# Performance work log

Measured on AMD Instinct MI355X. Metric: run time of the kernel, lower is better.

The kernel has to match this reference:

```python
import jax, jax.numpy as jnp
import numpy as np

# Dimensions (see shape_source): n_head == M == 8 is required by the module's own reshapes.
H = 8       # n_head
M = 8       # hardcoded M (must equal n_head)
D = 1024    # input_dim
E = 1024    # embed_dim
V = 128     # v_dim = embed_dim // n_head
KD = 128    # k_dim = v_dim
S = 10      # global seq_len == n_query (forced by delta_proj in-features)
K = 3       # K_num sampling points
HI, WI = 16, 16   # h_img, w_img feature-map size
BN = 4      # batch_n = batch_size // (h*w)
B = BN * HI * WI  # 1024
BNM = BN * M      # 32


def setup_inputs() -> dict:
    key = jax.random.key(0)
    ks = jax.random.split(key, 7)
    sc = 0.02
    return {
        "q": jax.random.normal(ks[0], (B, S, D), jnp.float32),
        "Wq": jax.random.normal(ks[1], (H, D, KD), jnp.float32) * sc,
        "Wk": jax.random.normal(ks[2], (H, D, KD), jnp.float32) * sc,
        "Wv": jax.random.normal(ks[3], (H, D, V * K), jnp.float32) * sc,
        "Wo": jax.random.normal(ks[4], (H, V, E), jnp.float32) * sc,
        "dw": jax.random.normal(ks[5], (2 * K * S, V * S), jnp.float32) * 0.01,
        "db": jax.random.uniform(ks[6], (2 * K * S,), jnp.float32, -1.0, 1.0),
    }


def _grid_sample_bilinear(feats, gx, gy):
    # Replicates F.grid_sample(mode='bilinear', padding_mode='zeros', align_corners=False)
    # feats: (N, h, w, S, V); gx, gy: (N, h, w, S, K) normalized grid coords in [-1, 1]-space
    n, h, w = feats.shape[0], feats.shape[1], feats.shape[2]
    ix = ((gx + 1.0) * w - 1.0) * 0.5  # unnormalize, align_corners=False
    iy = ((gy + 1.0) * h - 1.0) * 0.5
    x0 = jnp.floor(ix); y0 = jnp.floor(iy)
    x1 = x0 + 1.0;      y1 = y0 + 1.0
    wx1 = ix - x0; wx0 = 1.0 - wx1
    wy1 = iy - y0; wy0 = 1.0 - wy1
    b_idx = jnp.arange(n)[:, None, None, None, None]
    s_idx = jnp.arange(feats.shape[3])[None, None, None, :, None]

    def corner(xc, yc, wgt):
        xi = jnp.clip(xc.astype(jnp.int32), 0, w - 1)
        yi = jnp.clip(yc.astype(jnp.int32), 0, h - 1)
        valid = (xc >= 0) & (xc <= w - 1) & (yc >= 0) & (yc <= h - 1)
        val = feats[b_idx, yi, xi, s_idx]  # (N, h, w, S, K, V)
        return val * (wgt * valid)[..., None]

    return (corner(x0, y0, wx0 * wy0) + corner(x1, y0, wx1 * wy0)
            + corner(x0, y1, wx0 * wy1) + corner(x1, y1, wx1 * wy1))


def _l2norm_dim1(x):
    # F.normalize(x, p=2, dim=1) with eps=1e-12 (normalizes over the h axis)
    n = jnp.sqrt(jnp.sum(x * x, axis=1, keepdims=True))
    return x / jnp.maximum(n, 1e-12)


def _forward(q, Wq, Wk, Wv, Wo, dw, db):
    hf = q.reshape(-1, D)                                    # [B*S, D] (h defaults to q)
    qp = jnp.einsum('nd,hdk->hnk', hf, Wq).reshape(H, B, S, KD)
    kp = jnp.einsum('nd,hdk->hnk', hf, Wk).reshape(H, B, S, KD)
    vp = jnp.einsum('nd,hdk->hnk', hf, Wv).reshape(H, B, S * K, V)

    # torch: q.permute(1,2,3,0).contiguous().view(H, B, -1)  (memory reinterpretation)
    q2 = jnp.transpose(qp, (1, 2, 3, 0)).reshape(H, B, S * KD)

    deltas = (q2 @ dw.T + db).reshape(BNM, HI, WI, S, K, 2)

    gy, gx = jnp.meshgrid(jnp.arange(HI) / (HI - 1), jnp.arange(WI) / (WI - 1), indexing='ij')
    ref = jnp.stack((gx, gy), axis=-1).astype(q.dtype)        # (h, w, 2)

    pd = ref[None, :, :, None, None, :] + deltas              # (BNM, h, w, S, K, 2)
    vgx = _l2norm_dim1(pd[..., 0])
    vgy = _l2norm_dim1(pd[..., 1])

    feats = kp.reshape(BNM, HI, WI, S, V)                     # torch view of (H,B,S,k)
    samp = _grid_sample_bilinear(feats, vgx, vgy)             # (BNM, h, w, S, K, V)
    # torch stacks loop results at index k*S + s on a trailing dim, then permutes channels last
    samp = jnp.transpose(samp, (0, 1, 2, 4, 3, 5)).reshape(BNM, HI, WI, K * S, V)
    k_attn = samp.reshape(M, B, K * S, V)

    q_attn = q2.reshape(M, B, S, V)
    qk = jnp.einsum('mbqv,mbkv->mbqk', q_attn, k_attn) * (1.0 / np.sqrt(KD))
    attn = jax.nn.softmax(qk, axis=-1)                        # (M, B, S, K*S)
    attn_map = attn.mean(axis=0)[:, 0]                        # (B, K*S)

    head = jnp.einsum('mbqk,mbkv->mbqv', attn, vp)            # (M, B, S, V)
    head_flat = jnp.transpose(head, (1, 2, 0, 3)).reshape(B * S, H * V)
    out = (head_flat @ Wo.reshape(H * V, E)).reshape(B, S, E)
    return out, attn_map


def reference(q, Wq, Wk, Wv, Wo, dw, db):
    return _forward(q, Wq, Wk, Wv, Wo, dw, db)
```

## Files before the change

kernel.cpp:

```cpp
#include <hip/hip_runtime.h>


typedef float    f32x4 __attribute__((ext_vector_type(4)));
typedef short    s16x8 __attribute__((ext_vector_type(8)));
typedef unsigned short u16x8 __attribute__((ext_vector_type(8)));
typedef unsigned short u16;

__device__ __forceinline__ u16 f2bf(float f) {
  union { float f; unsigned u; } x; x.f = f;
  unsigned r = x.u + 0x7FFFu + ((x.u >> 16) & 1u);
  return (u16)(r >> 16);
}
__device__ __forceinline__ float bf2f(u16 u) {
  union { unsigned u; float f; } x; x.u = ((unsigned)u) << 16;
  return x.f;
}

#define ASYNC16(g, l) __builtin_amdgcn_global_load_lds(                       \
    (const __attribute__((address_space(1))) void*)(g),                       \
    (__attribute__((address_space(3))) void*)(l), 16, 0, 0)

__global__ __launch_bounds__(256) void conv_a(
    const float* __restrict__ src, u16* __restrict__ dst, int n8)
{
  int i = blockIdx.x * 256 + threadIdx.x;
  if (i >= n8) return;
  const float4* s = (const float4*)src + (size_t)i * 2;
  float4 a = s[0], b = s[1];
  u16x8 o;
  o[0] = f2bf(a.x); o[1] = f2bf(a.y); o[2] = f2bf(a.z); o[3] = f2bf(a.w);
  o[4] = f2bf(b.x); o[5] = f2bf(b.y); o[6] = f2bf(b.z); o[7] = f2bf(b.w);
  *(u16x8*)(dst + (size_t)i * 8) = o;
}

__global__ __launch_bounds__(256) void conv_w(
    const float* __restrict__ Wq, const float* __restrict__ Wk,
    const float* __restrict__ Wv, const float* __restrict__ Wo,
    u16* __restrict__ Wcat)
{
  int i = blockIdx.x * 256 + threadIdx.x;
  if (i >= 6144 * 128) return;
  int c = i >> 7;
  int d0 = (i & 127) * 8;
  const float* src; int stride;
  if (c < 1024)      { int kq = c >> 3, h = c & 7;
                       src = Wq + (size_t)h * 131072 + kq;      stride = 128; }
  else if (c < 2048) { int j = c - 1024; int h = j >> 7, k = j & 127;
                       src = Wk + (size_t)h * 131072 + k;       stride = 128; }
  else if (c < 5120) { int j = c - 2048; int h = j / 384, cc = j - h * 384;
                       src = Wv + (size_t)h * 393216 + cc;      stride = 384; }
  else               { int e = c - 5120;
                       src = Wo + e;                            stride = 1024; }
  u16x8 o;
#pragma unroll
  for (int r = 0; r < 8; ++r) o[r] = f2bf(src[(size_t)(d0 + r) * stride]);
  *(u16x8*)(Wcat + (size_t)c * 1024 + d0) = o;
}

__global__ __launch_bounds__(256) void conv_dw(
    const float* __restrict__ dw, u16* __restrict__ dwbf)
{
  int i = blockIdx.x * 256 + threadIdx.x;
  if (i >= 10240) return;
  int row = i / 160, ch = i - row * 160;
  int srow = (row < 60) ? row : 0;
  const float4* s = (const float4*)(dw + (size_t)srow * 1280 + ch * 8);
  float4 a = s[0], b = s[1];
  u16x8 o;
  o[0] = f2bf(a.x); o[1] = f2bf(a.y); o[2] = f2bf(a.z); o[3] = f2bf(a.w);
  o[4] = f2bf(b.x); o[5] = f2bf(b.y); o[6] = f2bf(b.z); o[7] = f2bf(b.w);
  *(u16x8*)(dwbf + (size_t)row * 1280 + ch * 8) = o;
}

template<int OUTBF>
__global__ __launch_bounds__(512, 2) void gemm_256(
    const u16* __restrict__ A, const u16* __restrict__ Bt,
    void* __restrict__ Cv, int ldc)
{
  extern __shared__ __align__(16) char smem[];
  const int tid = threadIdx.x;
  const int l   = tid & 63;
  const int wid = tid >> 6;
  const int wm  = wid >> 2;
  const int wn  = wid & 3;
  const int row0 = blockIdx.x * 256;
  const int col0 = blockIdx.y * 256;

  size_t goff[2]; int doff[2];
#pragma unroll
  for (int j = 0; j < 2; ++j) {
    int c = j * 512 + tid;
    int drow = c >> 3;
    int sg = (c & 7) ^ (drow & 7);
    goff[j] = (size_t)(drow * 2 + (sg >> 2)) * 1024 + (sg & 3) * 8;
    doff[j] = c * 16;
  }
  const u16* Agb = A  + (size_t)row0 * 1024;
  const u16* Bgb = Bt + (size_t)col0 * 1024;

#define STG(mtx, kh, tt, dd) do {                                             \
    const u16* sb_ = (mtx) ? Bgb : Agb;                                       \
    char* lb_ = smem + ((mtx) ? 65536 : 0) + (dd) * 32768 + (kh) * 16384;     \
    ASYNC16(sb_ + goff[0] + (tt) * 64 + (kh) * 32, lb_ + doff[0]);            \
    ASYNC16(sb_ + goff[1] + (tt) * 64 + (kh) * 32, lb_ + doff[1]);            \
  } while (0)

  const int lrow = l & 15, lk = l >> 4;
  const int p = (((lrow & 1) << 2) | lk) ^ ((lrow >> 1) & 7);
  const int rofs = (lrow >> 1) * 128 + p * 16;

  f32x4 acc[8][4];
#pragma unroll
  for (int i = 0; i < 8; ++i)
#pragma unroll
    for (int j = 0; j < 4; ++j) acc[i][j] = (f32x4){0.f, 0.f, 0.f, 0.f};

#define WAITV(n) asm volatile("s_waitcnt vmcnt(" #n ")" ::: "memory")
#define WAITL    asm volatile("s_waitcnt lgkmcnt(0)" ::: "memory")
#define SB       __builtin_amdgcn_sched_barrier(0)
#define BAR      __builtin_amdgcn_s_barrier()

  STG(0, 0, 0, 0); STG(1, 0, 0, 0);
  STG(0, 1, 0, 0); STG(1, 1, 0, 0);
  WAITV(4);
  BAR;
  SB;

  for (int t = 0; t < 16; ++t) {
    const int d = t & 1;
    const char* Abase = smem + d * 32768;
    const char* Bbase = smem + 65536 + d * 32768;
    s16x8 aR[8], bR[4];

#pragma unroll
    for (int kh = 0; kh < 2; ++kh) {
      const char* Ab = Abase + kh * 16384 + wm * 8192;
      const char* Bb = Bbase + kh * 16384 + wn * 4096;

#pragma unroll
      for (int fm = 0; fm < 4; ++fm)
        aR[fm] = *(const s16x8*)(Ab + fm * 1024 + rofs);
#pragma unroll
      for (int fn = 0; fn < 4; ++fn)
        bR[fn] = *(const s16x8*)(Bb + fn * 1024 + rofs);
      if (t < 15) STG(0, kh, t + 1, d ^ 1);
      SB; BAR;
      WAITL; SB;
      __builtin_amdgcn_s_setprio(1);
#pragma unroll
      for (int fm = 0; fm < 4; ++fm)
#pragma unroll
        for (int fn = 0; fn < 4; ++fn)
          acc[fm][fn] = __builtin_amdgcn_mfma_f32_16x16x32_bf16(
              aR[fm], bR[fn], acc[fm][fn], 0, 0, 0);
      __builtin_amdgcn_s_setprio(0);
      SB; BAR;

#pragma unroll
      for (int fm = 4; fm < 8; ++fm)
        aR[fm] = *(const s16x8*)(Ab + fm * 1024 + rofs);
      if (t < 15) STG(1, kh, t + 1, d ^ 1);
      SB; BAR;
      WAITL; SB;
      __builtin_amdgcn_s_setprio(1);
#pragma unroll
      for (int fm = 4; fm < 8; ++fm)
#pragma unroll
        for (int fn = 0; fn < 4; ++fn)
          acc[fm][fn] = __builtin_amdgcn_mfma_f32_16x16x32_bf16(
              aR[fm], bR[fn], acc[fm][fn], 0, 0, 0);
      __builtin_amdgcn_s_setprio(0);
      if (kh == 0) {
        if (t == 15) WAITV(0); else WAITV(4);
      } else {
        if (t < 15) WAITV(4);
      }
      SB; BAR;
    }
  }
#undef STG

  const int crow = l >> 4, ccol = l & 15;
#pragma unroll
  for (int fm = 0; fm < 8; ++fm)
#pragma unroll
    for (int fn = 0; fn < 4; ++fn) {
      size_t rb = (size_t)(row0 + wm * 128 + fm * 16 + crow * 4);
      int col = col0 + wn * 64 + fn * 16 + ccol;
      if (OUTBF) {
        u16* C = (u16*)Cv;
#pragma unroll
        for (int r = 0; r < 4; ++r)
          C[(rb + r) * ldc + col] = f2bf(acc[fm][fn][r]);
      } else {
        float* C = (float*)Cv;
#pragma unroll
        for (int r = 0; r < 4; ++r)
          C[(rb + r) * ldc + col] = acc[fm][fn][r];
      }
    }
}

__global__ __launch_bounds__(256) void delta_mfma(
    const u16* __restrict__ proj, const u16* __restrict__ dwbf,
    const float* __restrict__ db, float* __restrict__ deltas)
{
  __shared__ __align__(16) u16 As[64 * 32];
  __shared__ __align__(16) u16 Bs[64 * 32];
  const int tid  = threadIdx.x;
  const int lane = tid & 63;
  const int w    = tid >> 6;
  const int row0 = blockIdx.x * 64;
  const int wr   = w * 16;
  const int lrow = lane & 15;
  const int lk   = lane >> 4;

  f32x4 acc[4];
#pragma unroll
  for (int j = 0; j < 4; ++j) acc[j] = (f32x4){0.f, 0.f, 0.f, 0.f};

  const size_t lin0 = (size_t)(row0 + (tid >> 2)) * 1280 + (tid & 3) * 8;
  const u16* Bg = dwbf + (size_t)(tid >> 2) * 1280 + (tid & 3) * 8;
  char* AsB = (char*)As;  char* BsB = (char*)Bs;
  char* aL = AsB + w * 1024;
  char* bL = BsB + w * 1024;

  const int aoff = (wr + lrow) * 64 + lk * 16;
  int boff[4];
#pragma unroll
  for (int f = 0; f < 4; ++f) boff[f] = (f * 16 + lrow) * 64 + lk * 16;

  for (int k0 = 0; k0 < 1280; k0 += 32) {
    if (k0) __syncthreads();
    size_t lin = lin0 + k0;
    ASYNC16(proj + (lin >> 10) * 5120 + (lin & 1023), aL);
    ASYNC16(Bg + k0, bL);
    asm volatile("s_waitcnt vmcnt(0)" ::: "memory");
    __syncthreads();

    s16x8 af = *(const s16x8*)(AsB + aoff);
#pragma unroll
    for (int fn = 0; fn < 4; ++fn) {
      s16x8 bfr = *(const s16x8*)(BsB + boff[fn]);
      acc[fn] = __builtin_amdgcn_mfma_f32_16x16x32_bf16(af, bfr, acc[fn], 0, 0, 0);
    }
  }

  const int crow = lane >> 4;
  const int ccol = lane & 15;
#pragma unroll
  for (int fn = 0; fn < 4; ++fn) {
    int col = fn * 16 + ccol;
    if (col < 60) {
      float d = db[col];
      size_t rb = (size_t)(row0 + wr + crow * 4);
#pragma unroll
      for (int r = 0; r < 4; ++r)
        deltas[(rb + r) * 60 + col] = acc[fn][r] + d;
    }
  }
}

__global__ void coords_kernel(const float* __restrict__ deltas,
                              float* __restrict__ vgx, float* __restrict__ vgy)
{
  int g = blockIdx.x * 256 + threadIdx.x;
  if (g >= 32 * 16 * 10 * 3) return;
  int kk = g % 3, tmp = g / 3;
  int s = tmp % 10; tmp /= 10;
  int wi = tmp % 16; int bnm = tmp / 16;
  float gxr = wi * (1.0f / 15.0f);
  float px[16], py[16];
  float sx = 0.f, sy = 0.f;
#pragma unroll
  for (int hi = 0; hi < 16; ++hi) {
    size_t base = ((size_t)((bnm * 16 + hi) * 16 + wi)) * 60 + (s * 3 + kk) * 2;
    float x = gxr + deltas[base];
    float y = hi * (1.0f / 15.0f) + deltas[base + 1];
    px[hi] = x; py[hi] = y;
    sx += x * x; sy += y * y;
  }
  float rx = 1.0f / fmaxf(sqrtf(sx), 1e-12f);
  float ry = 1.0f / fmaxf(sqrtf(sy), 1e-12f);
#pragma unroll
  for (int hi = 0; hi < 16; ++hi) {
    size_t o = ((size_t)((bnm * 16 + hi) * 16 + wi) * 10 + s) * 3 + kk;
    vgx[o] = px[hi] * rx;
    vgy[o] = py[hi] * ry;
  }
}

__global__ __launch_bounds__(256) void attn_mfma(
    const u16* __restrict__ proj, const float* __restrict__ vgx,
    const float* __restrict__ vgy, u16* __restrict__ headf,
    float* __restrict__ attn0)
{
  const int bid = blockIdx.x;
  const int m = bid >> 10, b = bid & 1023;
  const int tid = threadIdx.x;
  const int lane = tid & 63;
  const int w = tid >> 6;

  __shared__ __align__(16) u16 ksb[32][136];
  __shared__ __align__(16) u16 vt[128][32];
  __shared__ __align__(16) u16 pl[16][40];
  __shared__ float wst[30][4];
  __shared__ int   cst[30][4];

  s16x8 aq[4];
  if (w == 0) {
    size_t linb = (size_t)bid * 1280 + (size_t)(lane & 15) * 128 + (lane >> 4) * 8;
#pragma unroll
    for (int kk = 0; kk < 4; ++kk) {
      size_t lin = linb + kk * 32;
      aq[kk] = *(const s16x8*)(proj + (lin >> 10) * 5120 + (lin & 1023));
    }
  }

  if (tid < 30) {
    int t = tid, kk = t / 10, sk = t % 10;
    size_t ci = ((size_t)bid * 10 + sk) * 3 + kk;
    float gx = vgx[ci], gy = vgy[ci];
    float ix = (gx + 1.0f) * 8.0f - 0.5f;
    float iy = (gy + 1.0f) * 8.0f - 0.5f;
    float x0f = floorf(ix), y0f = floorf(iy);
    float wx1 = ix - x0f, wx0 = 1.0f - wx1;
    float wy1 = iy - y0f, wy0 = 1.0f - wy1;
    float x1f = x0f + 1.0f, y1f = y0f + 1.0f;
    bool vx0 = (x0f >= 0.f) && (x0f <= 15.f);
    bool vx1 = (x1f >= 0.f) && (x1f <= 15.f);
    bool vy0 = (y0f >= 0.f) && (y0f <= 15.f);
    bool vy1 = (y1f >= 0.f) && (y1f <= 15.f);
    int x0 = min(max((int)x0f, 0), 15);
    int x1 = min(max((int)x1f, 0), 15);
    int y0 = min(max((int)y0f, 0), 15);
    int y1 = min(max((int)y1f, 0), 15);
    wst[t][0] = wx0 * wy0 * ((vx0 && vy0) ? 1.f : 0.f);
    wst[t][1] = wx1 * wy0 * ((vx1 && vy0) ? 1.f : 0.f);
    wst[t][2] = wx0 * wy1 * ((vx0 && vy1) ? 1.f : 0.f);
    wst[t][3] = wx1 * wy1 * ((vx1 && vy1) ? 1.f : 0.f);
    cst[t][0] = x0; cst[t][1] = x1; cst[t][2] = y0; cst[t][3] = y1;
  }
  __syncthreads();

  for (int i = tid; i < 512; i += 256) {
    int t = i & 31, c = i >> 5;
    u16x8 v = (u16x8){0, 0, 0, 0, 0, 0, 0, 0};
    if (t < 30) {
      int sv = t / 3, cv = t - sv * 3;
      v = *(const u16x8*)(proj + ((size_t)(b * 10 + sv)) * 5120 + 2048 +
                          m * 384 + cv * 128 + c * 8);
    }
#pragma unroll
    for (int r = 0; r < 8; ++r)
      vt[8 * c + r][t ^ (8 * (r & 3))] = v[r];
  }

  {
    int pb = (b >> 8) << 8;
    for (int i = tid; i < 480; i += 256) {
      int t = i >> 4, c = i & 15;
      int sk = t % 10;
      int x0 = cst[t][0], x1 = cst[t][1], y0 = cst[t][2], y1 = cst[t][3];
      float w00 = wst[t][0], w10 = wst[t][1], w01 = wst[t][2], w11 = wst[t][3];
      size_t colo = 1024 + (size_t)m * 128 + c * 8;
      const u16x8 f00 = *(const u16x8*)&proj[((size_t)((pb + y0 * 16 + x0) * 10 + sk)) * 5120 + colo];
      const u16x8 f10 = *(const u16x8*)&proj[((size_t)((pb + y0 * 16 + x1) * 10 + sk)) * 5120 + colo];
      const u16x8 f01 = *(const u16x8*)&proj[((size_t)((pb + y1 * 16 + x0) * 10 + sk)) * 5120 + colo];
      const u16x8 f11 = *(const u16x8*)&proj[((size_t)((pb + y1 * 16 + x1) * 10 + sk)) * 5120 + colo];
      u16x8 o;
#pragma unroll
      for (int r = 0; r < 8; ++r) {
        float acc = w00 * bf2f(f00[r]) + w10 * bf2f(f10[r]) +
                    w01 * bf2f(f01[r]) + w11 * bf2f(f11[r]);
        o[r] = f2bf(acc);
      }
      *(u16x8*)&ksb[t][c * 8] = o;
    }
  }
  __syncthreads();

  if (w == 0) {
    f32x4 dq[2];
    dq[0] = (f32x4){0.f, 0.f, 0.f, 0.f};
    dq[1] = (f32x4){0.f, 0.f, 0.f, 0.f};
    const int lr = lane & 15, g = lane >> 4;
#pragma unroll
    for (int kk = 0; kk < 4; ++kk) {
      s16x8 b0 = *(const s16x8*)&ksb[lr][g * 8 + kk * 32];
      s16x8 b1 = *(const s16x8*)&ksb[16 + lr][g * 8 + kk * 32];
      dq[0] = __builtin_amdgcn_mfma_f32_16x16x32_bf16(aq[kk], b0, dq[0], 0, 0, 0);
      dq[1] = __builtin_amdgcn_mfma_f32_16x16x32_bf16(aq[kk], b1, dq[1], 0, 0, 0);
    }
    float p[2][4];
#pragma unroll
    for (int f = 0; f < 2; ++f) {
      int t = lr + 16 * f;
#pragma unroll
      for (int r = 0; r < 4; ++r) {
        float v = dq[f][r] * 0.08838834764831845f;
        p[f][r] = (t < 30) ? v : -1e30f;
      }
    }
#pragma unroll
    for (int r = 0; r < 4; ++r) {
      float mx = fmaxf(p[0][r], p[1][r]);
#pragma unroll
      for (int msk = 1; msk <= 8; msk <<= 1) mx = fmaxf(mx, __shfl_xor(mx, msk));
      float e0 = __expf(p[0][r] - mx);
      float e1 = __expf(p[1][r] - mx);
      float sm = e0 + e1;
#pragma unroll
      for (int msk = 1; msk <= 8; msk <<= 1) sm += __shfl_xor(sm, msk);
      float inv = 1.0f / sm;
      p[0][r] = e0 * inv;
      p[1][r] = e1 * inv;
    }
    if (g == 0) {
      attn0[(size_t)bid * 30 + lr] = p[0][0];
      if (lr < 14) attn0[(size_t)bid * 30 + 16 + lr] = p[1][0];
    }
#pragma unroll
    for (int f = 0; f < 2; ++f)
#pragma unroll
      for (int r = 0; r < 4; ++r)
        pl[g * 4 + r][lr + 16 * f] = f2bf(p[f][r]);
  }
  __syncthreads();

  const int lr = lane & 15, g = lane >> 4;
  s16x8 pa = *(const s16x8*)&pl[lr][g * 8];
#pragma unroll
  for (int qf = 0; qf < 2; ++qf) {
    int fv = w * 2 + qf;
    int v = fv * 16 + lr;
    s16x8 bv = *(const s16x8*)&vt[v][8 * (g ^ (v & 3))];
    f32x4 acc = (f32x4){0.f, 0.f, 0.f, 0.f};
    acc = __builtin_amdgcn_mfma_f32_16x16x32_bf16(pa, bv, acc, 0, 0, 0);
#pragma unroll
    for (int r = 0; r < 4; ++r) {
      int s = g * 4 + r;
      if (s < 10)
        headf[((size_t)(b * 10 + s)) * 1024 + m * 128 + v] = f2bf(acc[r]);
    }
  }
}

__global__ void attnmap_kernel(const float* __restrict__ attn0, float* __restrict__ outa)
{
  int i = blockIdx.x * 256 + threadIdx.x;
  if (i >= 30720) return;
  int b = i / 30, t = i % 30;
  float s = 0.f;
  for (int mm = 0; mm < 8; ++mm) s += attn0[((size_t)mm * 1024 + b) * 30 + t];
  outa[i] = 0.125f * s;
}

extern "C" void kernel_launch(void* const* d_in, const int* in_sizes, int n_in,
                              void* d_out, int out_size, void* d_ws, size_t ws_size,
                              hipStream_t stream)
{
  const float* q  = (const float*)d_in[0];
  const float* Wq = (const float*)d_in[1];
  const float* Wk = (const float*)d_in[2];
  const float* Wv = (const float*)d_in[3];
  const float* Wo = (const float*)d_in[4];
  const float* dw = (const float*)d_in[5];
  const float* db = (const float*)d_in[6];
  float* out = (float*)d_out;
  float* attn_out = out + 10485760;

  char* p = (char*)d_ws;
  u16*   Abf   = (u16*)p;   p += 20971520;
  u16*   Wcat  = (u16*)p;   p += 12582912;
  u16*   proj  = (u16*)p;   p += 104857600;
  u16*   headf = (u16*)p;   p += 20971520;
  u16*   dwbf  = (u16*)p;   p += 163840;
  float* dels  = (float*)p; p += 1966080;
  float* vgxp  = (float*)p; p += 983040;
  float* vgyp  = (float*)p; p += 983040;
  float* attn0 = (float*)p; p += 983040;

  conv_a<<<dim3(5120), dim3(256), 0, stream>>>(q, Abf, 1310720);
  conv_w<<<dim3(3072), dim3(256), 0, stream>>>(Wq, Wk, Wv, Wo, Wcat);
  conv_dw<<<dim3(40), dim3(256), 0, stream>>>(dw, dwbf);

  gemm_256<1><<<dim3(40, 20), dim3(512), 131072, stream>>>(Abf, Wcat, proj, 5120);

  delta_mfma<<<dim3(128), dim3(256), 0, stream>>>(proj, dwbf, db, dels);
  coords_kernel<<<dim3(60), dim3(256), 0, stream>>>(dels, vgxp, vgyp);
  attn_mfma<<<dim3(8192), dim3(256), 0, stream>>>(proj, vgxp, vgyp, headf, attn0);
  attnmap_kernel<<<dim3(120), dim3(256), 0, stream>>>(attn0, attn_out);

  gemm_256<0><<<dim3(40, 4), dim3(512), 131072, stream>>>(
      headf, Wcat + (size_t)5120 * 1024, out, 1024);
}
```

Measured before the change: 257.4 us.

## Add 320x320 triple-buffered projection GEMM and pipeline delta_mfma loads

Replaces the 256x256 projection GEMM with a new 320x320-tile kernel that loads A and B together into a three-stage LDS ring. The larger tile gives 512 blocks, which is meant to fit one even wave on 256 CUs at two blocks per CU, and it raises reuse per tile. The delta_mfma kernel is also changed to a four-buffer async prefetch pipeline, so it no longer waits on each load before computing. The risks are more register pressure from 50 accumulator tiles, which could spill, and tricky wait counts.

```diff
diff --git a/kernel.cpp b/kernel.cpp
--- a/kernel.cpp
+++ b/kernel.cpp
@@ -19,6 +19,9 @@
 #define ASYNC16(g, l) __builtin_amdgcn_global_load_lds(                       \
     (const __attribute__((address_space(1))) void*)(g),                       \
     (__attribute__((address_space(3))) void*)(l), 16, 0, 0)
+#define WAITV(n) asm volatile("s_waitcnt vmcnt(" #n ")" ::: "memory")
+#define SB       __builtin_amdgcn_sched_barrier(0)
+#define BAR      __builtin_amdgcn_s_barrier()
 
 __global__ __launch_bounds__(256) void conv_a(
     const float* __restrict__ src, u16* __restrict__ dst, int n8)
@@ -72,6 +75,99 @@
   *(u16x8*)(dwbf + (size_t)row * 1280 + ch * 8) = o;
 }
 
+__global__ __launch_bounds__(512, 2) void gemm_320(
+    const u16* __restrict__ base, long bOff, u16* __restrict__ C, int ldc)
+{
+  extern __shared__ __align__(16) char smem[];
+  const int tid = threadIdx.x;
+  const int l   = tid & 63;
+  const int wid = tid >> 6;
+  const int wm  = wid >> 2;
+  const int wn  = wid & 3;
+  const int row0 = blockIdx.x * 320;
+  const int col0 = blockIdx.y * 320;
+
+  int eoff[5];
+#pragma unroll
+  for (int j = 0; j < 5; ++j) {
+    int c = j * 512 + tid;
+    int mc = (c < 1280) ? c : c - 1280;
+    int rp = mc >> 3, s = mc & 7, gs = s ^ (rp & 7);
+    int grow = rp * 2 + (gs >> 2), gk = (gs & 3) * 8;
+    eoff[j] = (c < 1280) ? ((row0 + grow) * 1024 + gk)
+                         : (int)(bOff + (size_t)(col0 + grow) * 1024 + gk);
+  }
+
+#define STG320(tt, bb) do {                                                   \
+    _Pragma("unroll")                                                         \
+    for (int j_ = 0; j_ < 5; ++j_)                                            \
+      ASYNC16(base + eoff[j_] + (tt) * 32,                                    \
+              smem + (bb) * 40960 + (j_ * 512 + tid) * 16);                   \
+  } while (0)
+
+  const int lrow = l & 15, lk = l >> 4;
+  int aoff[10], boff[5];
+  {
+    int rowA = wm * 160 + lrow;
+    int rpA = rowA >> 1, odA = (rowA & 1) << 2;
+#pragma unroll
+    for (int fm = 0; fm < 10; ++fm) {
+      int rp = rpA + fm * 8;
+      aoff[fm] = rp * 128 + (((odA | lk) ^ (rp & 7)) * 16);
+    }
+    int rowB = wn * 80 + lrow;
+    int rpB = rowB >> 1, odB = (rowB & 1) << 2;
+#pragma unroll
+    for (int fn = 0; fn < 5; ++fn) {
+      int rp = rpB + fn * 8;
+      boff[fn] = 20480 + rp * 128 + (((odB | lk) ^ (rp & 7)) * 16);
+    }
+  }
+
+  f32x4 acc[10][5];
+#pragma unroll
+  for (int i = 0; i < 10; ++i)
+#pragma unroll
+    for (int j = 0; j < 5; ++j) acc[i][j] = (f32x4){0.f, 0.f, 0.f, 0.f};
+
+  STG320(0, 0); STG320(1, 1);
+  WAITV(5);
+  SB; BAR; SB;
+
+  for (int t = 0; t < 32; ++t) {
+    const int cb = t % 3;
+    if (t + 2 < 32) STG320(t + 2, (t + 2) % 3);
+    const char* Ab = smem + cb * 40960;
+    s16x8 bR[5];
+#pragma unroll
+    for (int fn = 0; fn < 5; ++fn) bR[fn] = *(const s16x8*)(Ab + boff[fn]);
+#pragma unroll
+    for (int fm = 0; fm < 10; ++fm) {
+      s16x8 aT = *(const s16x8*)(Ab + aoff[fm]);
+#pragma unroll
+      for (int fn = 0; fn < 5; ++fn)
+        acc[fm][fn] = __builtin_amdgcn_mfma_f32_16x16x32_bf16(
+            aT, bR[fn], acc[fm][fn], 0, 0, 0);
+    }
+    if (t + 2 < 32) { WAITV(5); }
+    else if (t == 30) { WAITV(0); }
+    SB; BAR; SB;
+  }
+#undef STG320
+
+  const int crow = l >> 4, ccol = l & 15;
+#pragma unroll
+  for (int fm = 0; fm < 10; ++fm)
+#pragma unroll
+    for (int fn = 0; fn < 5; ++fn) {
+      size_t rb = (size_t)(row0 + wm * 160 + fm * 16 + crow * 4);
+      int col = col0 + wn * 80 + fn * 16 + ccol;
+#pragma unroll
+      for (int r = 0; r < 4; ++r)
+        C[(rb + r) * ldc + col] = f2bf(acc[fm][fn][r]);
+    }
+}
+
 template<int OUTBF>
 __global__ __launch_bounds__(512, 2) void gemm_256(
     const u16* __restrict__ A, const u16* __restrict__ Bt,
@@ -115,16 +211,12 @@
 #pragma unroll
     for (int j = 0; j < 4; ++j) acc[i][j] = (f32x4){0.f, 0.f, 0.f, 0.f};
 
-#define WAITV(n) asm volatile("s_waitcnt vmcnt(" #n ")" ::: "memory")
-#define WAITL    asm volatile("s_waitcnt lgkmcnt(0)" ::: "memory")
-#define SB       __builtin_amdgcn_sched_barrier(0)
-#define BAR      __builtin_amdgcn_s_barrier()
+#define WAITL asm volatile("s_waitcnt lgkmcnt(0)" ::: "memory")
 
   STG(0, 0, 0, 0); STG(1, 0, 0, 0);
   STG(0, 1, 0, 0); STG(1, 1, 0, 0);
   WAITV(4);
-  BAR;
-  SB;
+  BAR; SB;
 
   for (int t = 0; t < 16; ++t) {
     const int d = t & 1;
@@ -136,7 +228,6 @@
     for (int kh = 0; kh < 2; ++kh) {
       const char* Ab = Abase + kh * 16384 + wm * 8192;
       const char* Bb = Bbase + kh * 16384 + wn * 4096;
-
 #pragma unroll
       for (int fm = 0; fm < 4; ++fm)
         aR[fm] = *(const s16x8*)(Ab + fm * 1024 + rofs);
@@ -188,15 +279,15 @@
       size_t rb = (size_t)(row0 + wm * 128 + fm * 16 + crow * 4);
       int col = col0 + wn * 64 + fn * 16 + ccol;
       if (OUTBF) {
-        u16* C = (u16*)Cv;
+        u16* Cq = (u16*)Cv;
 #pragma unroll
         for (int r = 0; r < 4; ++r)
-          C[(rb + r) * ldc + col] = f2bf(acc[fm][fn][r]);
+          Cq[(rb + r) * ldc + col] = f2bf(acc[fm][fn][r]);
       } else {
-        float* C = (float*)Cv;
+        float* Cf = (float*)Cv;
 #pragma unroll
         for (int r = 0; r < 4; ++r)
-          C[(rb + r) * ldc + col] = acc[fm][fn][r];
+          Cf[(rb + r) * ldc + col] = acc[fm][fn][r];
       }
     }
 }
@@ -205,8 +296,8 @@
     const u16* __restrict__ proj, const u16* __restrict__ dwbf,
     const float* __restrict__ db, float* __restrict__ deltas)
 {
-  __shared__ __align__(16) u16 As[64 * 32];
-  __shared__ __align__(16) u16 Bs[64 * 32];
+  __shared__ __align__(16) u16 As[4][64 * 32];
+  __shared__ __align__(16) u16 Bs[4][64 * 32];
   const int tid  = threadIdx.x;
   const int lane = tid & 63;
   const int w    = tid >> 6;
@@ -221,30 +312,38 @@
 
   const size_t lin0 = (size_t)(row0 + (tid >> 2)) * 1280 + (tid & 3) * 8;
   const u16* Bg = dwbf + (size_t)(tid >> 2) * 1280 + (tid & 3) * 8;
-  char* AsB = (char*)As;  char* BsB = (char*)Bs;
-  char* aL = AsB + w * 1024;
-  char* bL = BsB + w * 1024;
+
+#define STD(kk, bb) do {                                                      \
+    size_t lin_ = lin0 + (kk) * 32;                                           \
+    ASYNC16(proj + (lin_ >> 10) * 5120 + (lin_ & 1023),                       \
+            (char*)As + (bb) * 4096 + w * 1024);                              \
+    ASYNC16(Bg + (kk) * 32, (char*)Bs + (bb) * 4096 + w * 1024);              \
+  } while (0)
 
   const int aoff = (wr + lrow) * 64 + lk * 16;
   int boff[4];
 #pragma unroll
   for (int f = 0; f < 4; ++f) boff[f] = (f * 16 + lrow) * 64 + lk * 16;
 
-  for (int k0 = 0; k0 < 1280; k0 += 32) {
-    if (k0) __syncthreads();
-    size_t lin = lin0 + k0;
-    ASYNC16(proj + (lin >> 10) * 5120 + (lin & 1023), aL);
-    ASYNC16(Bg + k0, bL);
-    asm volatile("s_waitcnt vmcnt(0)" ::: "memory");
-    __syncthreads();
-
-    s16x8 af = *(const s16x8*)(AsB + aoff);
+  STD(0, 0); STD(1, 1); STD(2, 2);
+  WAITV(4);
+  SB; BAR; SB;
+
+  for (int k = 0; k < 40; ++k) {
+    const int bb = k & 3;
+    if (k + 3 < 40) STD(k + 3, (k + 3) & 3);
+    s16x8 af = *(const s16x8*)((const char*)As + bb * 4096 + aoff);
 #pragma unroll
     for (int fn = 0; fn < 4; ++fn) {
-      s16x8 bfr = *(const s16x8*)(BsB + boff[fn]);
+      s16x8 bfr = *(const s16x8*)((const char*)Bs + bb * 4096 + boff[fn]);
       acc[fn] = __builtin_amdgcn_mfma_f32_16x16x32_bf16(af, bfr, acc[fn], 0, 0, 0);
     }
-  }
+    if (k < 37)      { WAITV(4); }
+    else if (k == 37){ WAITV(2); }
+    else if (k == 38){ WAITV(0); }
+    SB; BAR; SB;
+  }
+#undef STD
 
   const int crow = lane >> 4;
   const int ccol = lane & 15;
@@ -485,7 +584,8 @@
   conv_w<<<dim3(3072), dim3(256), 0, stream>>>(Wq, Wk, Wv, Wo, Wcat);
   conv_dw<<<dim3(40), dim3(256), 0, stream>>>(dw, dwbf);
 
-  gemm_256<1><<<dim3(40, 20), dim3(512), 131072, stream>>>(Abf, Wcat, proj, 5120);
+  gemm_320<<<dim3(32, 16), dim3(512), 122880, stream>>>(
+      Abf, 10485760L, proj, 5120);
 
   delta_mfma<<<dim3(128), dim3(256), 0, stream>>>(proj, dwbf, db, dels);
   coords_kernel<<<dim3(60), dim3(256), 0, stream>>>(dels, vgxp, vgyp);
```

New measurement: 238.9 us. 1.08x faster.
